# Performance work log

Hardware: AMD Instinct MI355X
Metric: run time of the kernel (lower is better)

## Reference

```python
import jax, jax.numpy as jnp
import numpy as np

NUM_HEAD = 8
HEAD_DIM = 32
MAX_DIST = 128
RATIO = 4  # smooth_embedding_ratio


def setup_inputs() -> dict:
    key = jax.random.key(0)
    ks = jax.random.split(key, 8)
    B, L, C = 4, 2048, 64
    H, D, md = NUM_HEAD, HEAD_DIM, MAX_DIST
    Wsm = (2 * md + 1) // RATIO  # 64

    def g(k, shape, scale=0.05):
        return jax.random.normal(k, shape, dtype=jnp.float32) * scale

    return {
        "x": g(ks[0], (B, L, C), 1.0),
        "Wq": g(ks[1], (C, H * D)),
        "bq": jnp.zeros((H * D,), jnp.float32),
        "Wk": g(ks[2], (C, H * D)),
        "bk": jnp.zeros((H * D,), jnp.float32),
        "Wv": g(ks[3], (C, H)),
        "distance_pe": g(ks[4], (H, D, Wsm, 1)),
        "u_pe": g(ks[5], (H, 1, 1, D)),
        "v_pe": g(ks[6], (H, 1, 1, D)),
    }


def reference(x, Wq, bq, Wk, bk, Wv, distance_pe, u_pe, v_pe):
    H, D, md = NUM_HEAD, HEAD_DIM, MAX_DIST
    W = 2 * md + 1
    B, L, _ = x.shape

    # projections, split into heads: (H, B, L, D)
    q = (x @ Wq + bq).reshape(B, L, H, D).transpose(2, 0, 1, 3)
    k = (x @ Wk + bk).reshape(B, L, H, D).transpose(2, 0, 1, 3)
    v = jax.nn.sigmoid(x @ Wv).transpose(2, 0, 1)  # (H, B, L)

    # Banded (q+u) @ k^T without materializing the full LxL score matrix.
    # TF does matmul + diag_part(k=(-md, md)) + permute + double reverse, which
    # equals att[h,b,n,m] = <q_u[h,b,(L-1-n)-(m-md)], k[h,b,L-1-n]> (0 if OOB).
    q_u = q + u_pe  # (H, B, L, D)
    q_pad = jnp.pad(q_u, ((0, 0), (0, 0), (md, md), (0, 0)))  # zeros match diag_part padding

    def band_at(m):
        # q_pad[j + 2*md - m] == q_u[j - (m - md)] (zero when out of range)
        qs = jax.lax.dynamic_slice_in_dim(q_pad, 2 * md - m, L, axis=2)
        return jnp.einsum('hbld,hbld->hbl', qs, k)

    band = jax.lax.map(band_at, jnp.arange(W))  # (W, H, B, L)
    att = jnp.transpose(band, (1, 2, 3, 0))[:, :, ::-1, :]  # (H, B, L, W)

    # Smoothed distance PE: bilinear upsample width Wsm -> W (TF2 half-pixel centers)
    smooth_pe = jax.image.resize(distance_pe, (H, D, W, 1), method='linear')[..., 0]  # (H, D, W)
    att = att + jnp.einsum('hbld,hdw->hblw', q + v_pe, smooth_pe)

    att = jax.nn.softmax(att * (float(D) ** -0.5), axis=-1)
    att = att * v[..., None]  # sigmoid value gating

    out = att.sum(axis=2)  # global mode: reduce over data_length -> (H, B, W)
    return jnp.transpose(out, (1, 2, 0))  # (B, W, H)
```

## Files before the change

### kernel.cpp

```cpp
#include <hip/hip_runtime.h>
#include <hip/hip_cooperative_groups.h>
#include <math.h>

namespace cg = cooperative_groups;

#define NH 8
#define HD 32
#define MD 128
#define NW 257
#define NWP 272
#define WSM 64
#define NB 4
#define NL 2048
#define NC 64
#define NHD 256
#define SP 40
#define ROWS 128
#define WIN 384
#define WTS 72
#define SC2 0.2550928063161107f

#define NBLK 512

using bf16x8 = __attribute__((ext_vector_type(8))) short;
using f32x4  = __attribute__((ext_vector_type(4))) float;
using i32x4  = __attribute__((ext_vector_type(4))) int;

__device__ __forceinline__ unsigned cvtpk(float lo, float hi) {
  unsigned r;
  asm("v_cvt_pk_bf16_f32 %0, %1, %2" : "=v"(r) : "v"(lo), "v"(hi));
  return r;
}
__device__ __forceinline__ void stb(unsigned short* p, float f) {
  *p = (unsigned short)cvtpk(f, f);
}

__device__ __forceinline__ void phaseA_body(
    unsigned short* wt, int bid, int tid,
    const float* __restrict__ x,
    const float* __restrict__ Wq, const float* __restrict__ bq,
    const float* __restrict__ Wk, const float* __restrict__ bk,
    const float* __restrict__ Wv, const float* __restrict__ dpe,
    const float* __restrict__ u_pe, const float* __restrict__ v_pe,
    unsigned short* __restrict__ qu, unsigned short* __restrict__ qv,
    unsigned short* __restrict__ kb, float* __restrict__ vv,
    unsigned short* __restrict__ spt, float* __restrict__ out) {
  bf16x8 a0, a1;
  int c = 0, g = 0, g8 = 0, w = 0, b = 0, l0 = 0, cb = 0;
  bool isQ = true;

  if (tid < 256) {
    const int t = tid;
    const int l64 = t & 63;
    w = t >> 6;
    c = l64 & 15; g = l64 >> 4; g8 = g * 8;
    const int br = bid >> 2;
    const int c0 = (bid & 3) << 7;
    const int r0 = br << 6;
    b = r0 >> 11;
    l0 = r0 & (NL - 1);
    isQ = (c0 < 256);
    const float* Wsrc = isQ ? Wq : Wk;
    cb = isQ ? c0 : c0 - 256;

#pragma unroll
    for (int i = 0; i < 4; ++i) {
      const int flat = t + i * 256;
      const int col4 = flat & 31;
      const int kp = flat >> 5;
      const float4 w0 = *reinterpret_cast<const float4*>(Wsrc + (2 * kp) * NHD + cb + 4 * col4);
      const float4 w1 = *reinterpret_cast<const float4*>(Wsrc + (2 * kp + 1) * NHD + cb + 4 * col4);
      unsigned* wp = reinterpret_cast<unsigned*>(wt);
      wp[(4 * col4 + 0) * (WTS / 2) + kp] = cvtpk(w0.x, w1.x);
      wp[(4 * col4 + 1) * (WTS / 2) + kp] = cvtpk(w0.y, w1.y);
      wp[(4 * col4 + 2) * (WTS / 2) + kp] = cvtpk(w0.z, w1.z);
      wp[(4 * col4 + 3) * (WTS / 2) + kp] = cvtpk(w0.w, w1.w);
    }

    const float* xr = x + (size_t)(r0 + 16 * w + c) * NC;
    const float4 x00 = *reinterpret_cast<const float4*>(xr + g8);
    const float4 x01 = *reinterpret_cast<const float4*>(xr + g8 + 4);
    const float4 x10 = *reinterpret_cast<const float4*>(xr + 32 + g8);
    const float4 x11 = *reinterpret_cast<const float4*>(xr + 32 + g8 + 4);
    const i32x4 a0i = {(int)cvtpk(x00.x, x00.y), (int)cvtpk(x00.z, x00.w),
                       (int)cvtpk(x01.x, x01.y), (int)cvtpk(x01.z, x01.w)};
    const i32x4 a1i = {(int)cvtpk(x10.x, x10.y), (int)cvtpk(x10.z, x10.w),
                       (int)cvtpk(x11.x, x11.y), (int)cvtpk(x11.z, x11.w)};
    a0 = __builtin_bit_cast(bf16x8, a0i);
    a1 = __builtin_bit_cast(bf16x8, a1i);
  } else if (tid < 384) {
    const int k = tid - 256;
    const int j = k >> 3, hh = k & 7;
    const int row = bid * 16 + j;
    const float* xr = x + (size_t)row * NC;
    float a = 0.f;
#pragma unroll
    for (int c4 = 0; c4 < NC / 4; ++c4) {
      const float4 xv = *reinterpret_cast<const float4*>(xr + 4 * c4);
      a = fmaf(xv.x, Wv[(4 * c4 + 0) * NH + hh], a);
      a = fmaf(xv.y, Wv[(4 * c4 + 1) * NH + hh], a);
      a = fmaf(xv.z, Wv[(4 * c4 + 2) * NH + hh], a);
      a = fmaf(xv.w, Wv[(4 * c4 + 3) * NH + hh], a);
    }
    const int bb = row >> 11, ll = row & (NL - 1);
    vv[((size_t)hh * NB + bb) * NL + ll] = 1.f / (1.f + __expf(-a));
  } else {
    const int k = tid - 384;
    if (k < 17) {
      const int oz = bid * 17 + k;
      if (oz < NB * NW * NH) out[oz] = 0.f;
    }
#pragma unroll
    for (int it = 0; it < 2; ++it) {
      const int k2 = k + it * 128;
      const int idx = bid * 136 + k2;
      if (k2 < 136 && idx < NH * NWP * HD) {
        const int d = idx & 31;
        const int hm = idx >> 5;
        const int m = hm % NWP;
        const int h = hm / NWP;
        float val = 0.f;
        if (m < NW) {
          float tt = (m + 0.5f) * ((float)WSM / (float)NW) - 0.5f;
          tt = fminf(fmaxf(tt, 0.f), (float)(WSM - 1));
          const int i0 = (int)tt;
          const float f = tt - (float)i0;
          const int i1 = (i0 + 1 < WSM) ? i0 + 1 : WSM - 1;
          const float* bse = dpe + ((size_t)h * HD + d) * WSM;
          val = (bse[i0] * (1.f - f) + bse[i1] * f) * SC2;
        }
        stb(spt + idx, val);
      }
    }
  }

  __syncthreads();

  if (tid < 256) {
    f32x4 acc[8];
#pragma unroll
    for (int tt = 0; tt < 8; ++tt) acc[tt] = {0.f, 0.f, 0.f, 0.f};
#pragma unroll
    for (int tt = 0; tt < 8; ++tt) {
      const bf16x8 b0 = *reinterpret_cast<const bf16x8*>(&wt[(16 * tt + c) * WTS + g8]);
      const bf16x8 b1 = *reinterpret_cast<const bf16x8*>(&wt[(16 * tt + c) * WTS + 32 + g8]);
      acc[tt] = __builtin_amdgcn_mfma_f32_16x16x32_bf16(a0, b0, acc[tt], 0, 0, 0);
      acc[tt] = __builtin_amdgcn_mfma_f32_16x16x32_bf16(a1, b1, acc[tt], 0, 0, 0);
    }
#pragma unroll
    for (int tt = 0; tt < 8; ++tt) {
      const int col = cb + 16 * tt + c;
      const int h = col >> 5, d = col & 31;
      const size_t rowbase = (((size_t)h * NB + b) * NL + l0 + 16 * w) * HD + d;
      if (isQ) {
        const float bias = bq[col];
        const float uu = u_pe[col], vp = v_pe[col];
#pragma unroll
        for (int r = 0; r < 4; ++r) {
          const float val = acc[tt][r] + bias;
          stb(qu + rowbase + (size_t)(4 * g + r) * HD, val + uu);
          stb(qv + rowbase + (size_t)(4 * g + r) * HD, val + vp);
        }
      } else {
        const float bias = bk[col];
#pragma unroll
        for (int r = 0; r < 4; ++r)
          stb(kb + rowbase + (size_t)(4 * g + r) * HD, (acc[tt][r] + bias) * SC2);
      }
    }
  }
}

__device__ __forceinline__ void phaseB_body(
    unsigned short* qu_sh, int bid, int tid,
    const unsigned short* __restrict__ qu, const unsigned short* __restrict__ qv,
    const unsigned short* __restrict__ kb, const float* __restrict__ vv,
    const unsigned short* __restrict__ spt, float* __restrict__ out) {
  float* red = reinterpret_cast<float*>(qu_sh);

  const int tile = bid & 15;
  const int hb = bid >> 4;
  const int b = hb & (NB - 1);
  const int h = hb >> 2;
  const int n0 = tile << 7;
  const int jlo = NL - ROWS - n0;
  const int l = tid & 63;
  const int w = tid >> 6;
  const int c = l & 15;
  const int g = l >> 4;
  const int g8 = g * 8;

  const unsigned short* qu_h = qu + (size_t)hb * NL * HD;
  const unsigned short* qv_h = qv + (size_t)hb * NL * HD;
  const unsigned short* k_h  = kb + (size_t)hb * NL * HD;
  const unsigned short* sp_h = spt + (size_t)h * NWP * HD;
  const float* vv_h = vv + (size_t)hb * NL;

  const bf16x8 ak  = *reinterpret_cast<const bf16x8*>(k_h  + (size_t)(jlo + 16 * w + c) * HD + g8);
  const bf16x8 aqv = *reinterpret_cast<const bf16x8*>(qv_h + (size_t)(n0 + 127 - 16 * w - c) * HD + g8);
  const f32x4 v4 = *reinterpret_cast<const f32x4*>(vv_h + (n0 + 124 - 16 * w - 4 * g));

  const int wq0_blk = jlo - MD;
  i32x4 stq[3];
#pragma unroll
  for (int it = 0; it < 3; ++it) {
    const int p = tid + it * 512;
    const int gr = wq0_blk + (p >> 2);
    i32x4 val = {0, 0, 0, 0};
    if ((unsigned)gr < (unsigned)NL)
      val = *reinterpret_cast<const i32x4*>(qu_h + (size_t)gr * HD + (p & 3) * 8);
    stq[it] = val;
  }

  const f32x4 z4 = {0.f, 0.f, 0.f, 0.f};

  f32x4 s[17];
#pragma unroll
  for (int t = 0; t < 17; ++t) {
    const bf16x8 bsp = *reinterpret_cast<const bf16x8*>(sp_h + (size_t)(16 * t + c) * HD + g8);
    s[t] = __builtin_amdgcn_mfma_f32_16x16x32_bf16(aqv, bsp, z4, 0, 0, 0);
  }

#pragma unroll
  for (int it = 0; it < 3; ++it) {
    const int p = tid + it * 512;
    *reinterpret_cast<i32x4*>(&qu_sh[(p >> 2) * SP + (p & 3) * 8]) = stq[it];
  }
  __syncthreads();

  int sl[4]; bool cond[4];
#pragma unroll
  for (int r = 0; r < 4; ++r) {
    sl[r] = 16 * g + ((4 * g + r - c) & 15);
    cond[r] = (4 * g + r) >= c;
  }

  f32x4 shp;
#pragma unroll
  for (int U = 0; U <= 16; ++U) {
    const bf16x8 bqu = *reinterpret_cast<const bf16x8*>(&qu_sh[(16 * w + 16 * U + c) * SP + g8]);
    const f32x4 c1 = __builtin_amdgcn_mfma_f32_16x16x32_bf16(ak, bqu, z4, 0, 0, 0);
    f32x4 shc;
#pragma unroll
    for (int r = 0; r < 4; ++r) shc[r] = __shfl(c1[r], sl[r], 64);
    if (U == 0) {
#pragma unroll
      for (int r = 0; r < 4; ++r)
        s[16][r] = (c == 0) ? (s[16][r] + shc[r]) : -1e30f;
    } else {
#pragma unroll
      for (int r = 0; r < 4; ++r)
        s[16 - U][r] += cond[r] ? shc[r] : shp[r];
    }
    shp = shc;
  }

  float wgt[4];
#pragma unroll
  for (int r = 0; r < 4; ++r) {
    float sum = 0.f;
#pragma unroll
    for (int t = 0; t < 17; ++t) {
      const float p = exp2f(s[t][r]);
      s[t][r] = p;
      sum += p;
    }
#pragma unroll
    for (int off = 1; off < 16; off <<= 1) sum += __shfl_xor(sum, off, 16);
    wgt[r] = v4[3 - r] * __builtin_amdgcn_rcpf(sum);
  }

  __syncthreads();
#pragma unroll
  for (int t = 0; t < 17; ++t) {
    float y = s[t][0] * wgt[0] + s[t][1] * wgt[1] + s[t][2] * wgt[2] + s[t][3] * wgt[3];
    y += __shfl_xor(y, 16, 64);
    y += __shfl_xor(y, 32, 64);
    if (l < 16) red[w * NWP + 16 * t + c] = y;
  }
  __syncthreads();
  for (int m = tid; m < NW; m += 512) {
    float ssum = 0.f;
#pragma unroll
    for (int ww = 0; ww < 8; ++ww) ssum += red[ww * NWP + m];
    atomicAdd(&out[((size_t)b * NW + m) * NH + h], ssum);
  }
}

__global__ __launch_bounds__(512, 4) void fused_coop(
    const float* __restrict__ x,
    const float* __restrict__ Wq, const float* __restrict__ bq,
    const float* __restrict__ Wk, const float* __restrict__ bk,
    const float* __restrict__ Wv, const float* __restrict__ dpe,
    const float* __restrict__ u_pe, const float* __restrict__ v_pe,
    unsigned short* __restrict__ qu, unsigned short* __restrict__ qv,
    unsigned short* __restrict__ kb, float* __restrict__ vv,
    unsigned short* __restrict__ spt, float* __restrict__ out) {
  __shared__ __align__(16) unsigned short smem[WIN * SP];
  phaseA_body(smem, blockIdx.x, threadIdx.x, x, Wq, bq, Wk, bk, Wv, dpe, u_pe, v_pe,
              qu, qv, kb, vv, spt, out);
  __threadfence();
  cg::this_grid().sync();
  phaseB_body(smem, blockIdx.x, threadIdx.x, qu, qv, kb, vv, spt, out);
}

__global__ __launch_bounds__(512, 4) void phaseA_kernel(
    const float* __restrict__ x,
    const float* __restrict__ Wq, const float* __restrict__ bq,
    const float* __restrict__ Wk, const float* __restrict__ bk,
    const float* __restrict__ Wv, const float* __restrict__ dpe,
    const float* __restrict__ u_pe, const float* __restrict__ v_pe,
    unsigned short* __restrict__ qu, unsigned short* __restrict__ qv,
    unsigned short* __restrict__ kb, float* __restrict__ vv,
    unsigned short* __restrict__ spt, float* __restrict__ out) {
  __shared__ __align__(16) unsigned short smem[128 * WTS];
  phaseA_body(smem, blockIdx.x, threadIdx.x, x, Wq, bq, Wk, bk, Wv, dpe, u_pe, v_pe,
              qu, qv, kb, vv, spt, out);
}

__global__ __launch_bounds__(512, 4) void phaseB_kernel(
    const unsigned short* __restrict__ qu, const unsigned short* __restrict__ qv,
    const unsigned short* __restrict__ kb, const float* __restrict__ vv,
    const unsigned short* __restrict__ spt, float* __restrict__ out) {
  __shared__ __align__(16) unsigned short smem[WIN * SP];
  phaseB_body(smem, blockIdx.x, threadIdx.x, qu, qv, kb, vv, spt, out);
}

extern "C" void kernel_launch(void* const* d_in, const int* in_sizes, int n_in,
                              void* d_out, int out_size, void* d_ws, size_t ws_size,
                              hipStream_t stream) {
  const float* x = (const float*)d_in[0];
  const float* Wq = (const float*)d_in[1];
  const float* bq = (const float*)d_in[2];
  const float* Wk = (const float*)d_in[3];
  const float* bk = (const float*)d_in[4];
  const float* Wv = (const float*)d_in[5];
  const float* dpe = (const float*)d_in[6];
  const float* u_pe = (const float*)d_in[7];
  const float* v_pe = (const float*)d_in[8];
  float* out = (float*)d_out;

  const size_t qk_elems = (size_t)NH * NB * NL * HD;
  float* vv = (float*)d_ws;
  unsigned short* qu = (unsigned short*)(vv + (size_t)NH * NB * NL);
  unsigned short* qv = qu + qk_elems;
  unsigned short* kb = qv + qk_elems;
  unsigned short* spt = kb + qk_elems;

  int coopAttr = 0, numCU = 0, maxPerCU = 0;
  hipDeviceGetAttribute(&coopAttr, hipDeviceAttributeCooperativeLaunch, 0);
  hipDeviceGetAttribute(&numCU, hipDeviceAttributeMultiprocessorCount, 0);
  hipOccupancyMaxActiveBlocksPerMultiprocessor(&maxPerCU, (const void*)fused_coop, 512, 0);

  if (coopAttr && maxPerCU > 0 && (long)maxPerCU * numCU >= NBLK) {
    void* args[] = {(void*)&x, (void*)&Wq, (void*)&bq, (void*)&Wk, (void*)&bk,
                    (void*)&Wv, (void*)&dpe, (void*)&u_pe, (void*)&v_pe,
                    (void*)&qu, (void*)&qv, (void*)&kb, (void*)&vv, (void*)&spt,
                    (void*)&out};
    if (hipLaunchCooperativeKernel((const void*)fused_coop, dim3(NBLK), dim3(512),
                                   args, 0, stream) == hipSuccess)
      return;
  }

  hipLaunchKernelGGL(phaseA_kernel, dim3(NBLK), dim3(512), 0, stream,
                     x, Wq, bq, Wk, bk, Wv, dpe, u_pe, v_pe, qu, qv, kb, vv, spt, out);
  hipLaunchKernelGGL(phaseB_kernel, dim3(NBLK), dim3(512), 0, stream,
                     qu, qv, kb, vv, spt, out);
}
```

Baseline: 34.14 us.

## Replace cooperative grid-sync kernel with two launches, add MFMA priority and block swizzle

```diff
diff --git a/kernel.cpp b/kernel.cpp
--- a/kernel.cpp
+++ b/kernel.cpp
@@ -1,8 +1,5 @@
 #include <hip/hip_runtime.h>
-#include <hip/hip_cooperative_groups.h>
 #include <math.h>
-
-namespace cg = cooperative_groups;
 
 #define NH 8
 #define HD 32
@@ -35,8 +32,7 @@
   *p = (unsigned short)cvtpk(f, f);
 }
 
-__device__ __forceinline__ void phaseA_body(
-    unsigned short* wt, int bid, int tid,
+__global__ __launch_bounds__(512, 4) void phaseA_kernel(
     const float* __restrict__ x,
     const float* __restrict__ Wq, const float* __restrict__ bq,
     const float* __restrict__ Wk, const float* __restrict__ bk,
@@ -45,6 +41,10 @@
     unsigned short* __restrict__ qu, unsigned short* __restrict__ qv,
     unsigned short* __restrict__ kb, float* __restrict__ vv,
     unsigned short* __restrict__ spt, float* __restrict__ out) {
+  __shared__ __align__(16) unsigned short wt[128 * WTS];
+  const int bid = blockIdx.x;
+  const int tid = threadIdx.x;
+
   bf16x8 a0, a1;
   int c = 0, g = 0, g8 = 0, w = 0, b = 0, l0 = 0, cb = 0;
   bool isQ = true;
@@ -140,6 +140,7 @@
     f32x4 acc[8];
 #pragma unroll
     for (int tt = 0; tt < 8; ++tt) acc[tt] = {0.f, 0.f, 0.f, 0.f};
+    __builtin_amdgcn_s_setprio(1);
 #pragma unroll
     for (int tt = 0; tt < 8; ++tt) {
       const bf16x8 b0 = *reinterpret_cast<const bf16x8*>(&wt[(16 * tt + c) * WTS + g8]);
@@ -147,6 +148,7 @@
       acc[tt] = __builtin_amdgcn_mfma_f32_16x16x32_bf16(a0, b0, acc[tt], 0, 0, 0);
       acc[tt] = __builtin_amdgcn_mfma_f32_16x16x32_bf16(a1, b1, acc[tt], 0, 0, 0);
     }
+    __builtin_amdgcn_s_setprio(0);
 #pragma unroll
     for (int tt = 0; tt < 8; ++tt) {
       const int col = cb + 16 * tt + c;
@@ -171,12 +173,16 @@
   }
 }
 
-__device__ __forceinline__ void phaseB_body(
-    unsigned short* qu_sh, int bid, int tid,
+__global__ __launch_bounds__(512, 4) void phaseB_kernel(
     const unsigned short* __restrict__ qu, const unsigned short* __restrict__ qv,
     const unsigned short* __restrict__ kb, const float* __restrict__ vv,
     const unsigned short* __restrict__ spt, float* __restrict__ out) {
+  __shared__ __align__(16) unsigned short qu_sh[WIN * SP];
   float* red = reinterpret_cast<float*>(qu_sh);
+
+  const int raw = blockIdx.x;
+  const int bid = (raw & 7) * 64 + (raw >> 3);
+  const int tid = threadIdx.x;
 
   const int tile = bid & 15;
   const int hb = bid >> 4;
@@ -215,11 +221,13 @@
   const f32x4 z4 = {0.f, 0.f, 0.f, 0.f};
 
   f32x4 s[17];
+  __builtin_amdgcn_s_setprio(1);
 #pragma unroll
   for (int t = 0; t < 17; ++t) {
     const bf16x8 bsp = *reinterpret_cast<const bf16x8*>(sp_h + (size_t)(16 * t + c) * HD + g8);
     s[t] = __builtin_amdgcn_mfma_f32_16x16x32_bf16(aqv, bsp, z4, 0, 0, 0);
   }
+  __builtin_amdgcn_s_setprio(0);
 
 #pragma unroll
   for (int it = 0; it < 3; ++it) {
@@ -236,6 +244,7 @@
   }
 
   f32x4 shp;
+  __builtin_amdgcn_s_setprio(1);
 #pragma unroll
   for (int U = 0; U <= 16; ++U) {
     const bf16x8 bqu = *reinterpret_cast<const bf16x8*>(&qu_sh[(16 * w + 16 * U + c) * SP + g8]);
@@ -254,6 +263,7 @@
     }
     shp = shc;
   }
+  __builtin_amdgcn_s_setprio(0);
 
   float wgt[4];
 #pragma unroll
@@ -285,45 +295,6 @@
     for (int ww = 0; ww < 8; ++ww) ssum += red[ww * NWP + m];
     atomicAdd(&out[((size_t)b * NW + m) * NH + h], ssum);
   }
-}
-
-__global__ __launch_bounds__(512, 4) void fused_coop(
-    const float* __restrict__ x,
-    const float* __restrict__ Wq, const float* __restrict__ bq,
-    const float* __restrict__ Wk, const float* __restrict__ bk,
-    const float* __restrict__ Wv, const float* __restrict__ dpe,
-    const float* __restrict__ u_pe, const float* __restrict__ v_pe,
-    unsigned short* __restrict__ qu, unsigned short* __restrict__ qv,
-    unsigned short* __restrict__ kb, float* __restrict__ vv,
-    unsigned short* __restrict__ spt, float* __restrict__ out) {
-  __shared__ __align__(16) unsigned short smem[WIN * SP];
-  phaseA_body(smem, blockIdx.x, threadIdx.x, x, Wq, bq, Wk, bk, Wv, dpe, u_pe, v_pe,
-              qu, qv, kb, vv, spt, out);
-  __threadfence();
-  cg::this_grid().sync();
-  phaseB_body(smem, blockIdx.x, threadIdx.x, qu, qv, kb, vv, spt, out);
-}
-
-__global__ __launch_bounds__(512, 4) void phaseA_kernel(
-    const float* __restrict__ x,
-    const float* __restrict__ Wq, const float* __restrict__ bq,
-    const float* __restrict__ Wk, const float* __restrict__ bk,
-    const float* __restrict__ Wv, const float* __restrict__ dpe,
-    const float* __restrict__ u_pe, const float* __restrict__ v_pe,
-    unsigned short* __restrict__ qu, unsigned short* __restrict__ qv,
-    unsigned short* __restrict__ kb, float* __restrict__ vv,
-    unsigned short* __restrict__ spt, float* __restrict__ out) {
-  __shared__ __align__(16) unsigned short smem[128 * WTS];
-  phaseA_body(smem, blockIdx.x, threadIdx.x, x, Wq, bq, Wk, bk, Wv, dpe, u_pe, v_pe,
-              qu, qv, kb, vv, spt, out);
-}
-
-__global__ __launch_bounds__(512, 4) void phaseB_kernel(
-    const unsigned short* __restrict__ qu, const unsigned short* __restrict__ qv,
-    const unsigned short* __restrict__ kb, const float* __restrict__ vv,
-    const unsigned short* __restrict__ spt, float* __restrict__ out) {
-  __shared__ __align__(16) unsigned short smem[WIN * SP];
-  phaseB_body(smem, blockIdx.x, threadIdx.x, qu, qv, kb, vv, spt, out);
 }
 
 extern "C" void kernel_launch(void* const* d_in, const int* in_sizes, int n_in,
@@ -347,21 +318,6 @@
   unsigned short* kb = qv + qk_elems;
   unsigned short* spt = kb + qk_elems;
 
-  int coopAttr = 0, numCU = 0, maxPerCU = 0;
-  hipDeviceGetAttribute(&coopAttr, hipDeviceAttributeCooperativeLaunch, 0);
-  hipDeviceGetAttribute(&numCU, hipDeviceAttributeMultiprocessorCount, 0);
-  hipOccupancyMaxActiveBlocksPerMultiprocessor(&maxPerCU, (const void*)fused_coop, 512, 0);
-
-  if (coopAttr && maxPerCU > 0 && (long)maxPerCU * numCU >= NBLK) {
-    void* args[] = {(void*)&x, (void*)&Wq, (void*)&bq, (void*)&Wk, (void*)&bk,
-                    (void*)&Wv, (void*)&dpe, (void*)&u_pe, (void*)&v_pe,
-                    (void*)&qu, (void*)&qv, (void*)&kb, (void*)&vv, (void*)&spt,
-                    (void*)&out};
-    if (hipLaunchCooperativeKernel((const void*)fused_coop, dim3(NBLK), dim3(512),
-                                   args, 0, stream) == hipSuccess)
-      return;
-  }
-
   hipLaunchKernelGGL(phaseA_kernel, dim3(NBLK), dim3(512), 0, stream,
                      x, Wq, bq, Wk, bk, Wv, dpe, u_pe, v_pe, qu, qv, kb, vv, spt, out);
   hipLaunchKernelGGL(phaseB_kernel, dim3(NBLK), dim3(512), 0, stream,
```

Result: no change. 33.90 us (-0.7%).
